# Optimization experiments

Measured on AMD Instinct MI355X. Metric: run time of the kernel, lower is better.

The kernel has to match this reference:

```python
import jax, jax.numpy as jnp
import numpy as np

N_HEADS = 8
MAX_TOP_K = 32
B, SQ, SKV, D_EMBED, D_CROSS = 8, 2048, 1024, 512, 768


def setup_inputs() -> dict:
    key = jax.random.key(0)
    ks = jax.random.split(key, 10)
    s = 0.02
    return {
        "x": jax.random.normal(ks[0], (B, SQ, D_EMBED), jnp.float32),
        "y": jax.random.normal(ks[1], (B, SKV, D_CROSS), jnp.float32),
        "wq": jax.random.normal(ks[2], (D_EMBED, D_EMBED), jnp.float32) * s,
        "bq": jnp.zeros((D_EMBED,), jnp.float32),
        "wk": jax.random.normal(ks[3], (D_EMBED, D_CROSS), jnp.float32) * s,
        "bk": jnp.zeros((D_EMBED,), jnp.float32),
        "wv": jax.random.normal(ks[4], (D_EMBED, D_CROSS), jnp.float32) * s,
        "bv": jnp.zeros((D_EMBED,), jnp.float32),
        "wo": jax.random.normal(ks[5], (D_EMBED, D_EMBED), jnp.float32) * s,
        "bo": jnp.zeros((D_EMBED,), jnp.float32),
    }


def _dynamic_sparse_topk(w, max_top_k):
    # w: [b,h,q,k] row-stochastic attention weights
    entropy = -(w * jnp.log(w + 1e-8)).sum(axis=-1, keepdims=True)  # [b,h,q,1]
    # torch .int() truncates toward zero, then clamp to [1, max_top_k]
    top_k = jnp.clip((max_top_k * (1.0 - entropy)).astype(jnp.int32), 1, max_top_k)
    sorted_w = -jnp.sort(-w, axis=-1)  # descending sort per row
    thresholds = jnp.take_along_axis(sorted_w, top_k - 1, axis=-1)  # [b,h,q,1]
    sparse = jnp.where(w >= thresholds, w, jnp.zeros_like(w))
    return sparse / (sparse.sum(axis=-1, keepdims=True) + 1e-8)


def reference(x, y, wq, bq, wk, bk, wv, bv, wo, bo):
    b, sq, d_embed = x.shape
    skv = y.shape[1]
    d_head = d_embed // N_HEADS
    q = (x @ wq.T + bq).reshape(b, sq, N_HEADS, d_head).transpose(0, 2, 1, 3)
    k = (y @ wk.T + bk).reshape(b, skv, N_HEADS, d_head).transpose(0, 2, 1, 3)
    v = (y @ wv.T + bv).reshape(b, skv, N_HEADS, d_head).transpose(0, 2, 1, 3)
    scale = 1.0 / np.sqrt(d_head).astype(np.float32)
    attn = jnp.einsum('bhqd,bhkd->bhqk', q, k) * scale
    attn = jax.nn.softmax(attn, axis=-1)
    attn = _dynamic_sparse_topk(attn, MAX_TOP_K)
    out = jnp.einsum('bhqk,bhkd->bhqd', attn, v)
    out = out.transpose(0, 2, 1, 3).reshape(b, sq, d_embed)
    return out @ wo.T + bo
```

## Files before the change

kernel.cpp:

```cpp
#include <hip/hip_runtime.h>
#include <cstdint>
#include <cmath>

#define DH 64
#define SQB 2048
#define SKVB 1024
#define DE 512

typedef _Float16 f16;
typedef _Float16 f16x8 __attribute__((ext_vector_type(8)));
typedef float f32x4 __attribute__((ext_vector_type(4)));
typedef float f32x16 __attribute__((ext_vector_type(16)));

#define MFMA32(A, B, C) __builtin_amdgcn_mfma_f32_32x32x16_f16(A, B, C, 0, 0, 0)

__global__ __launch_bounds__(256)
void split_f16(const float* __restrict__ in, f16* __restrict__ hi,
               f16* __restrict__ lo, int n4, float scale) {
  const int i = blockIdx.x * 256 + threadIdx.x;
  if (i >= n4) return;
  float4 v = ((const float4*)in)[i];
  v.x *= scale; v.y *= scale; v.z *= scale; v.w *= scale;
  f16 h0 = (f16)v.x, h1 = (f16)v.y, h2 = (f16)v.z, h3 = (f16)v.w;
  f16 l0 = (f16)(v.x - (float)h0), l1 = (f16)(v.y - (float)h1);
  f16 l2 = (f16)(v.z - (float)h2), l3 = (f16)(v.w - (float)h3);
  f16 hb[4] = {h0, h1, h2, h3};
  f16 lb[4] = {l0, l1, l2, l3};
  ((uint2*)hi)[i] = *(const uint2*)hb;
  ((uint2*)lo)[i] = *(const uint2*)lb;
}

template <int NSPLIT, int OUT>
__global__ __launch_bounds__(256, 2)
void gemm_f16(const f16* __restrict__ Ah, const f16* __restrict__ Al,
              const f16* __restrict__ Wh, const f16* __restrict__ Wl,
              const float* __restrict__ bias, float* __restrict__ C,
              f16* __restrict__ Ch, f16* __restrict__ Cl,
              int M, int N, int K, float inv, float oscale) {
  __shared__ f16 smem[(NSPLIT == 3 ? 4 : 2) * 4096];
  f16* As  = smem;
  f16* Als = (NSPLIT == 3) ? smem + 4096 : nullptr;
  f16* Ws  = smem + (NSPLIT == 3 ? 8192 : 4096);
  f16* Wls = (NSPLIT == 3) ? smem + 12288 : nullptr;

  const int tid = threadIdx.x;
  const int w = tid >> 6;
  const int l = tid & 63;
  const int wm = w >> 1, wn = w & 1;
  const int m0 = blockIdx.y * 128;
  const int n0 = blockIdx.x * 128;

  const int srow = tid >> 2;
  const int schk = tid & 3;
  const f16* pA  = Ah + (size_t)(m0 + srow) * K + schk * 8;
  const f16* pW  = Wh + (size_t)(n0 + srow) * K + schk * 8;
  const f16* pAl = (NSPLIT == 3) ? Al + (size_t)(m0 + srow) * K + schk * 8 : nullptr;
  const f16* pWl = (NSPLIT == 3) ? Wl + (size_t)(n0 + srow) * K + schk * 8 : nullptr;
  const size_t rowskip = (size_t)64 * K;

  const int d0 = srow * 32 + ((schk ^ (srow & 3)) * 8);
  const int fbase = (l & 15) * 32 + (((l >> 4) ^ (l & 3)) * 8);
  const int fA = wm * 2048 + fbase;
  const int fW = wn * 2048 + fbase;

  f32x4 acc[4][4] = {};
  uint4 rA0, rA1, rW0, rW1, rAl0, rAl1, rWl0, rWl1;

  rA0 = *(const uint4*)(pA);            rA1 = *(const uint4*)(pA + rowskip);
  rW0 = *(const uint4*)(pW);            rW1 = *(const uint4*)(pW + rowskip);
  if constexpr (NSPLIT == 3) {
    rAl0 = *(const uint4*)(pAl);        rAl1 = *(const uint4*)(pAl + rowskip);
    rWl0 = *(const uint4*)(pWl);        rWl1 = *(const uint4*)(pWl + rowskip);
  }

  for (int k0 = 0; k0 < K; k0 += 32) {
    __syncthreads();
    *(uint4*)&As[d0] = rA0;  *(uint4*)&As[d0 + 2048] = rA1;
    *(uint4*)&Ws[d0] = rW0;  *(uint4*)&Ws[d0 + 2048] = rW1;
    if constexpr (NSPLIT == 3) {
      *(uint4*)&Als[d0] = rAl0;  *(uint4*)&Als[d0 + 2048] = rAl1;
      *(uint4*)&Wls[d0] = rWl0;  *(uint4*)&Wls[d0 + 2048] = rWl1;
    }
    __syncthreads();

    if (k0 + 32 < K) {
      rA0 = *(const uint4*)(pA + k0 + 32);  rA1 = *(const uint4*)(pA + rowskip + k0 + 32);
      rW0 = *(const uint4*)(pW + k0 + 32);  rW1 = *(const uint4*)(pW + rowskip + k0 + 32);
      if constexpr (NSPLIT == 3) {
        rAl0 = *(const uint4*)(pAl + k0 + 32); rAl1 = *(const uint4*)(pAl + rowskip + k0 + 32);
        rWl0 = *(const uint4*)(pWl + k0 + 32); rWl1 = *(const uint4*)(pWl + rowskip + k0 + 32);
      }
    }

    f16x8 ah[4], wh[4], al[4], wl[4];
#pragma unroll
    for (int i = 0; i < 4; ++i) ah[i] = *(const f16x8*)&As[fA + i * 512];
#pragma unroll
    for (int j = 0; j < 4; ++j) wh[j] = *(const f16x8*)&Ws[fW + j * 512];
    if constexpr (NSPLIT == 3) {
#pragma unroll
      for (int i = 0; i < 4; ++i) al[i] = *(const f16x8*)&Als[fA + i * 512];
#pragma unroll
      for (int j = 0; j < 4; ++j) wl[j] = *(const f16x8*)&Wls[fW + j * 512];
    }

#pragma unroll
    for (int i = 0; i < 4; ++i)
#pragma unroll
      for (int j = 0; j < 4; ++j)
        acc[i][j] = __builtin_amdgcn_mfma_f32_16x16x32_f16(ah[i], wh[j], acc[i][j], 0, 0, 0);
    if constexpr (NSPLIT == 3) {
#pragma unroll
      for (int i = 0; i < 4; ++i)
#pragma unroll
        for (int j = 0; j < 4; ++j)
          acc[i][j] = __builtin_amdgcn_mfma_f32_16x16x32_f16(ah[i], wl[j], acc[i][j], 0, 0, 0);
#pragma unroll
      for (int i = 0; i < 4; ++i)
#pragma unroll
        for (int j = 0; j < 4; ++j)
          acc[i][j] = __builtin_amdgcn_mfma_f32_16x16x32_f16(al[i], wh[j], acc[i][j], 0, 0, 0);
    }
  }

  const int rr = (l >> 4) * 4;
  const int cc = l & 15;
#pragma unroll
  for (int j = 0; j < 4; ++j) {
    const int n = n0 + wn * 64 + j * 16 + cc;
    const float bv = bias[n];
#pragma unroll
    for (int i = 0; i < 4; ++i) {
      const int m = m0 + wm * 64 + i * 16 + rr;
#pragma unroll
      for (int r = 0; r < 4; ++r) {
        const float val = acc[i][j][r] * inv + bv;
        if constexpr (OUT == 0) {
          C[(size_t)(m + r) * N + n] = val;
        } else {
          const float sv = val * oscale;
          const f16 hh = (f16)sv;
          const f16 ll = (f16)(sv - (float)hh);
          Ch[(size_t)(m + r) * N + n] = hh;
          Cl[(size_t)(m + r) * N + n] = ll;
        }
      }
    }
  }
}

__device__ __forceinline__ f32x16 qk_accum(const f16x8 ah[4], const f16x8 al[4],
                                           const f16x8 qh_[4], const f16x8 ql_[4]) {
  f32x16 ca = (f32x16){};
  f32x16 cb = (f32x16){};
  ca = MFMA32(ah[0], qh_[0], ca);  cb = MFMA32(ah[1], qh_[1], cb);
  ca = MFMA32(ah[2], qh_[2], ca);  cb = MFMA32(ah[3], qh_[3], cb);
  ca = MFMA32(al[0], qh_[0], ca);  cb = MFMA32(al[1], qh_[1], cb);
  ca = MFMA32(al[2], qh_[2], ca);  cb = MFMA32(al[3], qh_[3], cb);
  ca = MFMA32(ah[0], ql_[0], ca);  cb = MFMA32(ah[1], ql_[1], cb);
  ca = MFMA32(ah[2], ql_[2], ca);  cb = MFMA32(ah[3], ql_[3], cb);
  return ca + cb;
}

__device__ __forceinline__ f32x16 qk_tile_global(const f16* __restrict__ kgh,
                                                 const f16* __restrict__ kgl,
                                                 int tt, int q5, int hi5,
                                                 const f16x8 qh_[4], const f16x8 ql_[4]) {
  const f16* kh = kgh + (size_t)(tt * 32 + q5) * DE + hi5 * 8;
  const f16* kl = kgl + (size_t)(tt * 32 + q5) * DE + hi5 * 8;
  f16x8 ah[4], al[4];
#pragma unroll
  for (int s = 0; s < 4; ++s) {
    ah[s] = *(const f16x8*)(kh + s * 16);
    al[s] = *(const f16x8*)(kl + s * 16);
  }
  return qk_accum(ah, al, qh_, ql_);
}

__global__ __launch_bounds__(256, 3)
void attn_v11(const f16* __restrict__ qhb, const f16* __restrict__ qlb,
              const f16* __restrict__ khb, const f16* __restrict__ klb,
              const float* __restrict__ vb, f16* __restrict__ ob) {
  __shared__ f16 Ks[2][2][4096];
  __shared__ float4 stat[4][32];
  __shared__ int   sidx[4][48];
  __shared__ float sp[4][48];
  __shared__ int   scnt[4][2];

  const int phys = blockIdx.x;
  const int bid = (phys & 7) * 128 + (phys >> 3);
  const int b  = bid >> 7;
  const int h  = (bid >> 4) & 7;
  const int qt = bid & 15;
  const int tid = threadIdx.x;
  const int w  = tid >> 6;
  const int l  = tid & 63;
  const int q5 = l & 31;
  const int hi5 = l >> 5;

  const float C2 = 1.44269504f / 4096.0f;

  const int qrow = qt * 128 + w * 32 + q5;
  const f16* qpb = qhb + (size_t)(b * SQB + qrow) * DE + h * DH + hi5 * 8;
  const f16* qpl = qlb + (size_t)(b * SQB + qrow) * DE + h * DH + hi5 * 8;
  f16x8 qh_[4], ql_[4];
#pragma unroll
  for (int s = 0; s < 4; ++s) {
    qh_[s] = *(const f16x8*)(qpb + s * 16);
    ql_[s] = *(const f16x8*)(qpl + s * 16);
  }

  const f16* kgh = khb + (size_t)(b * SKVB) * DE + h * DH;
  const f16* kgl = klb + (size_t)(b * SKVB) * DE + h * DH;

  const int skv0 = tid >> 3;
  const int sch  = tid & 7;
  const int d_off0 = skv0 * 64 + ((sch ^ (skv0 & 7)) * 8);
  const int d_off1 = (32 + skv0) * 64 + ((sch ^ (skv0 & 7)) * 8);

  {
    const f16* shp = kgh + (size_t)skv0 * DE + sch * 8;
    const f16* slp = kgl + (size_t)skv0 * DE + sch * 8;
    uint4 a0 = *(const uint4*)(shp);
    uint4 a1 = *(const uint4*)(shp + 32 * DE);
    uint4 b0 = *(const uint4*)(slp);
    uint4 b1 = *(const uint4*)(slp + 32 * DE);
    *(uint4*)&Ks[0][0][d_off0] = a0;
    *(uint4*)&Ks[0][0][d_off1] = a1;
    *(uint4*)&Ks[0][1][d_off0] = b0;
    *(uint4*)&Ks[0][1][d_off1] = b1;
  }
  __syncthreads();

  float m = -INFINITY, Z = 0.f, H = 0.f;
  int mt = 0;
  bool tie = false;
  f32x16 best = (f32x16){};

  for (int t = 0; t < 16; ++t) {
    const int cur = t & 1;
    const int nxt = cur ^ 1;
    uint4 La0, La1, Lb0, Lb1;
    const bool more = (t + 1 < 16);
    if (more) {
      const f16* shp = kgh + (size_t)((t + 1) * 64 + skv0) * DE + sch * 8;
      const f16* slp = kgl + (size_t)((t + 1) * 64 + skv0) * DE + sch * 8;
      La0 = *(const uint4*)(shp);
      La1 = *(const uint4*)(shp + 32 * DE);
      Lb0 = *(const uint4*)(slp);
      Lb1 = *(const uint4*)(slp + 32 * DE);
    }
#pragma unroll
    for (int u = 0; u < 2; ++u) {
      const int kvl = u * 32 + q5;
      const int rowoff = kvl * 64;
      f16x8 ah[4], al[4];
#pragma unroll
      for (int s = 0; s < 4; ++s) {
        const int idx = rowoff + (((s * 2 + hi5) ^ (q5 & 7)) * 8);
        ah[s] = *(const f16x8*)&Ks[cur][0][idx];
        al[s] = *(const f16x8*)&Ks[cur][1][idx];
      }
      const f32x16 sv = qk_accum(ah, al, qh_, ql_);
      float t0 = fmaxf(fmaxf(sv[0], sv[1]), fmaxf(sv[2], sv[3]));
      float t1 = fmaxf(fmaxf(sv[4], sv[5]), fmaxf(sv[6], sv[7]));
      float t2 = fmaxf(fmaxf(sv[8], sv[9]), fmaxf(sv[10], sv[11]));
      float t3 = fmaxf(fmaxf(sv[12], sv[13]), fmaxf(sv[14], sv[15]));
      const float tmax = fmaxf(fmaxf(t0, t1), fmaxf(t2, t3));
#pragma unroll
      for (int r = 0; r < 16; ++r) {
        const float s = sv[r];
        const float e = __builtin_amdgcn_exp2f(s * C2);
        Z += e;
        H = fmaf(e, s, H);
      }
      const bool upd = (tmax > m);
      tie = upd ? false : (tie || (tmax == m));
      if (upd) { m = tmax; mt = t * 2 + u; }
#pragma unroll
      for (int r = 0; r < 16; ++r) best[r] = upd ? sv[r] : best[r];
    }
    if (more) {
      *(uint4*)&Ks[nxt][0][d_off0] = La0;
      *(uint4*)&Ks[nxt][0][d_off1] = La1;
      *(uint4*)&Ks[nxt][1][d_off0] = Lb0;
      *(uint4*)&Ks[nxt][1][d_off1] = Lb1;
    }
    __syncthreads();
  }

  const float mo = __shfl_xor(m, 32);
  const int tieo = __shfl_xor(tie ? 1 : 0, 32);
  Z += __shfl_xor(Z, 32);
  H += __shfl_xor(H, 32);
  const float mc = fmaxf(m, mo);
  const bool tiec = (m > mo) ? tie : ((mo > m) ? (tieo != 0) : (tie || tieo != 0));

  int c = 0, p1 = -1, p2 = -1;
#pragma unroll
  for (int r = 0; r < 16; ++r) {
    if (best[r] == mc) {
      const int pos = mt * 32 + (r & 3) + 8 * (r >> 2) + 4 * hi5;
      p2 = (c == 1) ? pos : p2;
      p1 = (c == 0) ? pos : p1;
      ++c;
    }
  }
  const int co  = __shfl_xor(c, 32);
  const int p1o = __shfl_xor(p1, 32);
  const int p2o = __shfl_xor(p2, 32);
  const int ct = c + co;
  const int pa = (c > 0) ? p1 : p1o;
  const int pb = (c >= 2) ? p2 : ((c == 1) ? ((co > 0) ? p1o : -1)
                                           : ((co >= 2) ? p2o : -1));

  const float E = __logf(Z) - (H * (1.0f / 4096.0f)) / Z;
  int tk = (int)(32.0f * (1.0f - E));
  tk = tk < 1 ? 1 : (tk > 32 ? 32 : tk);
  const bool slowRow = (tk > 1) || tiec || (ct > 2);
  const float zeps = 1e-8f * Z * __builtin_amdgcn_exp2f(-mc * C2);
  const float wt = 1.0f / ((float)ct + zeps);

  if (hi5 == 0)
    stat[w][q5] = make_float4(slowRow ? -1.0f : wt,
                              __int_as_float(pa),
                              __int_as_float(ct == 2 ? pb : -1),
                              (float)ct);

  {
    const size_t obase = (size_t)(b * SQB + qt * 128 + w * 32) * DE + h * DH + l;
    const float* vB = vb + (size_t)(b * SKVB) * DE + h * DH + l;
    for (int r = 0; r < 32; ++r) {
      const float4 st = stat[w][r];
      if (st.x >= 0.f) {
        const int ppa = __float_as_int(st.y);
        const int ppb = __float_as_int(st.z);
        float acc = vB[(size_t)ppa * DE];
        if (ppb >= 0) acc += vB[(size_t)ppb * DE];
        ob[obase + (size_t)r * DE] = (f16)(acc * st.x);
      }
    }
  }

  {
    unsigned long long sb = __ballot(slowRow && hi5 == 0);
    while (sb != 0ull) {
      const int rr = (int)__builtin_ctzll(sb);
      sb &= sb - 1;
      const float mr = __shfl(mc, rr);
      const int tkr  = __shfl(tk, rr);
      const float Zr = __shfl(Z, rr);
      float thr = mr;
      float rem = (float)tkr;
      float cand = mr;
      int guard = 0;
      bool done = false;
      while (!done && guard < 40) {
        ++guard;
        float cf = 0.f, nmx = -INFINITY;
        for (int tt = 0; tt < 32; ++tt) {
          const f32x16 sv = qk_tile_global(kgh, kgl, tt, q5, hi5, qh_, ql_);
          if (q5 == rr) {
#pragma unroll
            for (int r = 0; r < 16; ++r) {
              cf += (sv[r] == cand) ? 1.f : 0.f;
              nmx = (sv[r] < cand) ? fmaxf(nmx, sv[r]) : nmx;
            }
          }
        }
        cf += __shfl_xor(cf, 32);
        nmx = fmaxf(nmx, __shfl_xor(nmx, 32));
        const float cfr = __shfl(cf, rr);
        const float nmr = __shfl(nmx, rr);
        if (cfr >= rem) { thr = cand; done = true; }
        else { rem -= cfr; cand = nmr; }
      }
      int myc = 0;
      for (int tt = 0; tt < 32; ++tt) {
        const f32x16 sv = qk_tile_global(kgh, kgl, tt, q5, hi5, qh_, ql_);
        if (q5 == rr) {
#pragma unroll
          for (int r = 0; r < 16; ++r) {
            if (sv[r] >= thr && myc < 24) {
              sidx[w][hi5 * 24 + myc] = tt * 32 + (r & 3) + 8 * (r >> 2) + 4 * hi5;
              sp[w][hi5 * 24 + myc] = __builtin_amdgcn_exp2f((sv[r] - mr) * C2);
              ++myc;
            }
          }
        }
      }
      if (q5 == rr) scnt[w][hi5] = myc;
      int c0 = scnt[w][0]; c0 = c0 > 24 ? 24 : c0;
      int c1 = scnt[w][1]; c1 = c1 > 24 ? 24 : c1;
      float acc = 0.f, ps = 0.f;
      const float* vB = vb + (size_t)(b * SKVB) * DE + h * DH + l;
      for (int e = 0; e < c0; ++e) {
        const int kv = sidx[w][e]; const float p = sp[w][e];
        ps += p; acc = fmaf(p, vB[(size_t)kv * DE], acc);
      }
      for (int e = 0; e < c1; ++e) {
        const int kv = sidx[w][24 + e]; const float p = sp[w][24 + e];
        ps += p; acc = fmaf(p, vB[(size_t)kv * DE], acc);
      }
      const float zepsr = 1e-8f * Zr * __builtin_amdgcn_exp2f(-mr * C2);
      const float o = acc / (ps + zepsr);
      ob[(size_t)(b * SQB + qt * 128 + w * 32 + rr) * DE + h * DH + l] = (f16)o;
    }
  }
}

extern "C" void kernel_launch(void* const* d_in, const int* in_sizes, int n_in,
                              void* d_out, int out_size, void* d_ws, size_t ws_size,
                              hipStream_t stream) {
  const float* x  = (const float*)d_in[0];
  const float* y  = (const float*)d_in[1];
  const float* wq = (const float*)d_in[2];
  const float* bq = (const float*)d_in[3];
  const float* wk = (const float*)d_in[4];
  const float* bk = (const float*)d_in[5];
  const float* wv = (const float*)d_in[6];
  const float* bv = (const float*)d_in[7];
  const float* wo = (const float*)d_in[8];
  const float* bo = (const float*)d_in[9];
  float* out = (float*)d_out;

  char* ws = (char*)d_ws;
  const size_t MiB = 1048576;

  f16* xh  = (f16*)(ws);
  f16* xl  = (f16*)(ws + 16 * MiB);
  f16* yh  = (f16*)(ws + 32 * MiB);
  f16* yl  = (f16*)(ws + 44 * MiB);
  f16* qh  = (f16*)(ws + 56 * MiB);
  f16* ql  = (f16*)(ws + 72 * MiB);
  f16* kh  = (f16*)(ws + 88 * MiB);
  f16* kl  = (f16*)(ws + 96 * MiB);
  float* v = (float*)(ws + 104 * MiB);
  f16* ao  = (f16*)(ws + 120 * MiB);
  f16* wqh = (f16*)(ws + 136 * MiB);
  f16* wql = (f16*)(ws + 136 * MiB + 524288);
  f16* wkh = (f16*)(ws + 137 * MiB);
  f16* wkl = (f16*)(ws + 137 * MiB + 786432);
  f16* wvh = (f16*)(ws + 138 * MiB + 524288);
  f16* wvl = (f16*)(ws + 139 * MiB + 262144);
  f16* woh = (f16*)(ws + 140 * MiB);
  f16* wol = (f16*)(ws + 140 * MiB + 524288);

  dim3 blk(256);
  const float WS = 2048.0f, IWS = 1.0f / 2048.0f;

  split_f16<<<dim3(8192), blk, 0, stream>>>(x, xh, xl, 2097152, 1.0f);
  split_f16<<<dim3(6144), blk, 0, stream>>>(y, yh, yl, 1572864, 1.0f);
  split_f16<<<dim3(256),  blk, 0, stream>>>(wq, wqh, wql, 65536, WS);
  split_f16<<<dim3(384),  blk, 0, stream>>>(wk, wkh, wkl, 98304, WS);
  split_f16<<<dim3(384),  blk, 0, stream>>>(wv, wvh, wvl, 98304, 1.0f);
  split_f16<<<dim3(256),  blk, 0, stream>>>(wo, woh, wol, 65536, 1.0f);

  gemm_f16<3, 1><<<dim3(4, 128), blk, 0, stream>>>(xh, xl, wqh, wql, bq,
      nullptr, qh, ql, 16384, 512, 512, IWS, 8.0f);
  gemm_f16<3, 1><<<dim3(4, 64), blk, 0, stream>>>(yh, yl, wkh, wkl, bk,
      nullptr, kh, kl, 8192, 512, 768, IWS, 64.0f);
  gemm_f16<1, 0><<<dim3(4, 64), blk, 0, stream>>>(yh, nullptr, wvh, nullptr, bv,
      v, nullptr, nullptr, 8192, 512, 768, 1.0f, 1.0f);

  attn_v11<<<dim3(1024), blk, 0, stream>>>(qh, ql, kh, kl, v, ao);

  gemm_f16<1, 0><<<dim3(4, 128), blk, 0, stream>>>(ao, nullptr, woh, nullptr, bo,
      out, nullptr, nullptr, 16384, 512, 512, 1.0f, 1.0f);
}
```

Before: 221.1 us.

## Use direct global-to-LDS double-buffered loads in GEMM and merge split launches

The GEMM main loop now issues global_load_lds copies straight into a double-buffered shared-memory tile for the next K step while MFMAs run on the current buffer. This removes the register staging and one barrier per iteration. The six fp32-to-f16 split kernels are also folded into two launches to cut launch overhead. Double buffering doubles LDS per block, which may reduce occupancy for the 3-split variant. The swizzled source addressing has to match the fragment read pattern.

After: 212.8 us. 3.7% less time.

```diff
diff --git a/kernel.cpp b/kernel.cpp
--- a/kernel.cpp
+++ b/kernel.cpp
@@ -11,14 +11,19 @@
 typedef _Float16 f16x8 __attribute__((ext_vector_type(8)));
 typedef float f32x4 __attribute__((ext_vector_type(4)));
 typedef float f32x16 __attribute__((ext_vector_type(16)));
+typedef unsigned int u32;
 
 #define MFMA32(A, B, C) __builtin_amdgcn_mfma_f32_32x32x16_f16(A, B, C, 0, 0, 0)
 
-__global__ __launch_bounds__(256)
-void split_f16(const float* __restrict__ in, f16* __restrict__ hi,
-               f16* __restrict__ lo, int n4, float scale) {
-  const int i = blockIdx.x * 256 + threadIdx.x;
-  if (i >= n4) return;
+__device__ __forceinline__ void gl16(const f16* g, f16* l) {
+  __builtin_amdgcn_global_load_lds(
+      (const __attribute__((address_space(1))) u32*)g,
+      (__attribute__((address_space(3))) u32*)l, 16, 0, 0);
+}
+
+__device__ __forceinline__ void do_split(const float* __restrict__ in,
+                                         f16* __restrict__ hi, f16* __restrict__ lo,
+                                         int i, float scale) {
   float4 v = ((const float4*)in)[i];
   v.x *= scale; v.y *= scale; v.z *= scale; v.w *= scale;
   f16 h0 = (f16)v.x, h1 = (f16)v.y, h2 = (f16)v.z, h3 = (f16)v.w;
@@ -30,6 +35,29 @@
   ((uint2*)lo)[i] = *(const uint2*)lb;
 }
 
+__global__ __launch_bounds__(256)
+void split2(const float* __restrict__ a, f16* __restrict__ ah, f16* __restrict__ al, int na,
+            const float* __restrict__ b, f16* __restrict__ bh, f16* __restrict__ bl, int nb) {
+  const int i = blockIdx.x * 256 + threadIdx.x;
+  if (i < na) do_split(a, ah, al, i, 1.0f);
+  else if (i < na + nb) do_split(b, bh, bl, i - na, 1.0f);
+}
+
+__global__ __launch_bounds__(256)
+void split4(const float* __restrict__ a, f16* __restrict__ ah, f16* __restrict__ al, int na, float sa,
+            const float* __restrict__ b, f16* __restrict__ bh, f16* __restrict__ bl, int nb, float sb,
+            const float* __restrict__ c, f16* __restrict__ ch, f16* __restrict__ cl, int nc, float sc,
+            const float* __restrict__ d, f16* __restrict__ dh, f16* __restrict__ dl, int nd, float sd) {
+  int i = blockIdx.x * 256 + threadIdx.x;
+  if (i < na) { do_split(a, ah, al, i, sa); return; }
+  i -= na;
+  if (i < nb) { do_split(b, bh, bl, i, sb); return; }
+  i -= nb;
+  if (i < nc) { do_split(c, ch, cl, i, sc); return; }
+  i -= nc;
+  if (i < nd) do_split(d, dh, dl, i, sd);
+}
+
 template <int NSPLIT, int OUT>
 __global__ __launch_bounds__(256, 2)
 void gemm_f16(const f16* __restrict__ Ah, const f16* __restrict__ Al,
@@ -37,11 +65,8 @@
               const float* __restrict__ bias, float* __restrict__ C,
               f16* __restrict__ Ch, f16* __restrict__ Cl,
               int M, int N, int K, float inv, float oscale) {
-  __shared__ f16 smem[(NSPLIT == 3 ? 4 : 2) * 4096];
-  f16* As  = smem;
-  f16* Als = (NSPLIT == 3) ? smem + 4096 : nullptr;
-  f16* Ws  = smem + (NSPLIT == 3 ? 8192 : 4096);
-  f16* Wls = (NSPLIT == 3) ? smem + 12288 : nullptr;
+  constexpr int NPART = (NSPLIT == 3) ? 4 : 2;
+  __shared__ f16 smem[2][NPART * 4096];
 
   const int tid = threadIdx.x;
   const int w = tid >> 6;
@@ -50,58 +75,66 @@
   const int m0 = blockIdx.y * 128;
   const int n0 = blockIdx.x * 128;
 
-  const int srow = tid >> 2;
-  const int schk = tid & 3;
-  const f16* pA  = Ah + (size_t)(m0 + srow) * K + schk * 8;
-  const f16* pW  = Wh + (size_t)(n0 + srow) * K + schk * 8;
-  const f16* pAl = (NSPLIT == 3) ? Al + (size_t)(m0 + srow) * K + schk * 8 : nullptr;
-  const f16* pWl = (NSPLIT == 3) ? Wl + (size_t)(n0 + srow) * K + schk * 8 : nullptr;
-  const size_t rowskip = (size_t)64 * K;
-
-  const int d0 = srow * 32 + ((schk ^ (srow & 3)) * 8);
+  const f16* gA  = Ah + (size_t)m0 * K;
+  const f16* gW  = Wh + (size_t)n0 * K;
+  const f16* gAl = (NSPLIT == 3) ? Al + (size_t)m0 * K : nullptr;
+  const f16* gWl = (NSPLIT == 3) ? Wl + (size_t)n0 * K : nullptr;
+
   const int fbase = (l & 15) * 32 + (((l >> 4) ^ (l & 3)) * 8);
   const int fA = wm * 2048 + fbase;
   const int fW = wn * 2048 + fbase;
 
+  const int s0   = w * 128 + l;
+  const int dl0  = (w * 128) * 8;
+  const int dl1  = (w * 128 + 64) * 8;
+
   f32x4 acc[4][4] = {};
-  uint4 rA0, rA1, rW0, rW1, rAl0, rAl1, rWl0, rWl1;
-
-  rA0 = *(const uint4*)(pA);            rA1 = *(const uint4*)(pA + rowskip);
-  rW0 = *(const uint4*)(pW);            rW1 = *(const uint4*)(pW + rowskip);
-  if constexpr (NSPLIT == 3) {
-    rAl0 = *(const uint4*)(pAl);        rAl1 = *(const uint4*)(pAl + rowskip);
-    rWl0 = *(const uint4*)(pWl);        rWl1 = *(const uint4*)(pWl + rowskip);
-  }
+
+  auto stage = [&](int k0, int bsel) {
+    {
+      const int s = s0;
+      const int srow = s >> 2;
+      const int koff = k0 + (((s & 3) ^ (srow & 3)) * 8);
+      const size_t go = (size_t)srow * K + koff;
+      gl16(gA + go, &smem[bsel][dl0]);
+      gl16(gW + go, &smem[bsel][4096 + dl0]);
+      if constexpr (NSPLIT == 3) {
+        gl16(gAl + go, &smem[bsel][8192 + dl0]);
+        gl16(gWl + go, &smem[bsel][12288 + dl0]);
+      }
+    }
+    {
+      const int s = s0 + 64;
+      const int srow = s >> 2;
+      const int koff = k0 + (((s & 3) ^ (srow & 3)) * 8);
+      const size_t go = (size_t)srow * K + koff;
+      gl16(gA + go, &smem[bsel][dl1]);
+      gl16(gW + go, &smem[bsel][4096 + dl1]);
+      if constexpr (NSPLIT == 3) {
+        gl16(gAl + go, &smem[bsel][8192 + dl1]);
+        gl16(gWl + go, &smem[bsel][12288 + dl1]);
+      }
+    }
+  };
+
+  stage(0, 0);
+  __syncthreads();
+  int buf = 0;
 
   for (int k0 = 0; k0 < K; k0 += 32) {
-    __syncthreads();
-    *(uint4*)&As[d0] = rA0;  *(uint4*)&As[d0 + 2048] = rA1;
-    *(uint4*)&Ws[d0] = rW0;  *(uint4*)&Ws[d0 + 2048] = rW1;
+    if (k0 + 32 < K) stage(k0 + 32, buf ^ 1);
+
+    const f16* Ls = smem[buf];
+    f16x8 ah[4], wh[4], al[4], wl[4];
+#pragma unroll
+    for (int i = 0; i < 4; ++i) ah[i] = *(const f16x8*)&Ls[fA + i * 512];
+#pragma unroll
+    for (int j = 0; j < 4; ++j) wh[j] = *(const f16x8*)&Ls[4096 + fW + j * 512];
     if constexpr (NSPLIT == 3) {
-      *(uint4*)&Als[d0] = rAl0;  *(uint4*)&Als[d0 + 2048] = rAl1;
-      *(uint4*)&Wls[d0] = rWl0;  *(uint4*)&Wls[d0 + 2048] = rWl1;
-    }
-    __syncthreads();
-
-    if (k0 + 32 < K) {
-      rA0 = *(const uint4*)(pA + k0 + 32);  rA1 = *(const uint4*)(pA + rowskip + k0 + 32);
-      rW0 = *(const uint4*)(pW + k0 + 32);  rW1 = *(const uint4*)(pW + rowskip + k0 + 32);
-      if constexpr (NSPLIT == 3) {
-        rAl0 = *(const uint4*)(pAl + k0 + 32); rAl1 = *(const uint4*)(pAl + rowskip + k0 + 32);
-        rWl0 = *(const uint4*)(pWl + k0 + 32); rWl1 = *(const uint4*)(pWl + rowskip + k0 + 32);
-      }
-    }
-
-    f16x8 ah[4], wh[4], al[4], wl[4];
-#pragma unroll
-    for (int i = 0; i < 4; ++i) ah[i] = *(const f16x8*)&As[fA + i * 512];
-#pragma unroll
-    for (int j = 0; j < 4; ++j) wh[j] = *(const f16x8*)&Ws[fW + j * 512];
-    if constexpr (NSPLIT == 3) {
-#pragma unroll
-      for (int i = 0; i < 4; ++i) al[i] = *(const f16x8*)&Als[fA + i * 512];
-#pragma unroll
-      for (int j = 0; j < 4; ++j) wl[j] = *(const f16x8*)&Wls[fW + j * 512];
+#pragma unroll
+      for (int i = 0; i < 4; ++i) al[i] = *(const f16x8*)&Ls[8192 + fA + i * 512];
+#pragma unroll
+      for (int j = 0; j < 4; ++j) wl[j] = *(const f16x8*)&Ls[12288 + fW + j * 512];
     }
 
 #pragma unroll
@@ -121,6 +154,8 @@
         for (int j = 0; j < 4; ++j)
           acc[i][j] = __builtin_amdgcn_mfma_f32_16x16x32_f16(al[i], wh[j], acc[i][j], 0, 0, 0);
     }
+    __syncthreads();
+    buf ^= 1;
   }
 
   const int rr = (l >> 4) * 4;
@@ -449,12 +484,12 @@
   dim3 blk(256);
   const float WS = 2048.0f, IWS = 1.0f / 2048.0f;
 
-  split_f16<<<dim3(8192), blk, 0, stream>>>(x, xh, xl, 2097152, 1.0f);
-  split_f16<<<dim3(6144), blk, 0, stream>>>(y, yh, yl, 1572864, 1.0f);
-  split_f16<<<dim3(256),  blk, 0, stream>>>(wq, wqh, wql, 65536, WS);
-  split_f16<<<dim3(384),  blk, 0, stream>>>(wk, wkh, wkl, 98304, WS);
-  split_f16<<<dim3(384),  blk, 0, stream>>>(wv, wvh, wvl, 98304, 1.0f);
-  split_f16<<<dim3(256),  blk, 0, stream>>>(wo, woh, wol, 65536, 1.0f);
+  split2<<<dim3(14336), blk, 0, stream>>>(x, xh, xl, 2097152,
+                                          y, yh, yl, 1572864);
+  split4<<<dim3(1280), blk, 0, stream>>>(wq, wqh, wql, 65536, WS,
+                                         wk, wkh, wkl, 98304, WS,
+                                         wv, wvh, wvl, 98304, 1.0f,
+                                         wo, woh, wol, 65536, 1.0f);
 
   gemm_f16<3, 1><<<dim3(4, 128), blk, 0, stream>>>(xh, xl, wqh, wql, bq,
       nullptr, qh, ql, 16384, 512, 512, IWS, 8.0f);
```
